# Kernel optimization log

Hardware: AMD Instinct MI355X
Metric: run time of the kernel (lower is better)

Reference implementation:

```python
import jax, jax.numpy as jnp
import numpy as np

TEMPERATURE = 0.5
EPS = 1e-8  # torch.nn.CosineSimilarity default eps


def setup_inputs() -> dict:
    key = jax.random.key(0)
    k1, k2 = jax.random.split(key)
    B, D = 4096, 256
    z1 = jax.random.normal(k1, (B, D), dtype=jnp.float32)
    # z2 = perturbed view of z1 so positive cosine sims are positive
    # (original torch code takes log of the RAW cosine sim, which is NaN
    #  for negative positives; realistic SimCLR positives are correlated views)
    z2 = z1 + 0.1 * jax.random.normal(k2, (B, D), dtype=jnp.float32)
    return {"z1": z1, "z2": z2}


def reference(z1, z2):
    B = z1.shape[0]
    z = jnp.concatenate([z1, z2], axis=0)                      # [2B, D]
    norm = jnp.maximum(jnp.linalg.norm(z, axis=-1, keepdims=True), EPS)
    zn = z / norm
    sim = zn @ zn.T                                            # [2B, 2B] cosine sims
    # positives: sim[i, i+B] and sim[i+B, i] (RAW cosine, per original code)
    pos = jnp.concatenate([jnp.diagonal(sim, offset=B),
                           jnp.diagonal(sim, offset=-B)])      # [2B]
    # mask self-similarity diagonal to -inf before exp-sum
    diag = jnp.eye(2 * B, dtype=bool)
    sim_masked = jnp.where(diag, -jnp.inf, sim)
    denom = jnp.sum(jnp.exp(sim_masked / TEMPERATURE), axis=-1)  # [2B]
    loss = -jnp.mean(jnp.log(pos / denom))
    return loss
```

## Files before the change

kernel.cpp:

```cpp
#include <hip/hip_runtime.h>
#include <hip/hip_bf16.h>


#define NROWS 8192
#define BHALF 4096
#define DDIM  256
#define CHUNK 4

typedef __attribute__((ext_vector_type(4))) int   i32x4;
typedef __attribute__((ext_vector_type(8))) int   i32x8;
typedef __attribute__((ext_vector_type(4))) float f32x4;

#define SCALE1 0x7F7F7F7F
#define TWO_LOG2E 2.8853900817779268f

__device__ __forceinline__ void load_lds16(const unsigned char* g, unsigned char* l) {
    __builtin_amdgcn_global_load_lds(
        (const __attribute__((address_space(1))) void*)g,
        (__attribute__((address_space(3))) void*)l, 16, 0, 0);
}

__global__ __launch_bounds__(256) void prep_kernel(const float* __restrict__ z1,
                                                   const float* __restrict__ z2,
                                                   unsigned char* __restrict__ zn8,
                                                   float* __restrict__ posPart,
                                                   float* __restrict__ denom,
                                                   float* __restrict__ out) {
    __shared__ float sp[4];
    int wave = threadIdx.x >> 6;
    int lane = threadIdx.x & 63;
    int i    = blockIdx.x * 4 + wave;
    float4 a = reinterpret_cast<const float4*>(z1 + (size_t)i * DDIM)[lane];
    float4 b = reinterpret_cast<const float4*>(z2 + (size_t)i * DDIM)[lane];
    float ss1 = a.x * a.x + a.y * a.y + a.z * a.z + a.w * a.w;
    float ss2 = b.x * b.x + b.y * b.y + b.z * b.z + b.w * b.w;
    float dd  = a.x * b.x + a.y * b.y + a.z * b.z + a.w * b.w;
    #pragma unroll
    for (int off = 32; off; off >>= 1) {
        ss1 += __shfl_xor(ss1, off);
        ss2 += __shfl_xor(ss2, off);
        dd  += __shfl_xor(dd, off);
    }
    float n1 = fmaxf(sqrtf(ss1), 1e-8f);
    float n2 = fmaxf(sqrtf(ss2), 1e-8f);
    float i1 = 1.0f / n1, i2 = 1.0f / n2;
    int pa = __builtin_amdgcn_cvt_pk_fp8_f32(a.x * i1, a.y * i1, 0, 0);
    pa     = __builtin_amdgcn_cvt_pk_fp8_f32(a.z * i1, a.w * i1, pa, 1);
    int pb = __builtin_amdgcn_cvt_pk_fp8_f32(b.x * i2, b.y * i2, 0, 0);
    pb     = __builtin_amdgcn_cvt_pk_fp8_f32(b.z * i2, b.w * i2, pb, 1);
    reinterpret_cast<int*>(zn8 + (size_t)i * DDIM)[lane] = pa;
    reinterpret_cast<int*>(zn8 + (size_t)(i + BHALF) * DDIM)[lane] = pb;
    if (lane == 0) sp[wave] = __logf(dd * i1 * i2);
    if (threadIdx.x < 8) denom[blockIdx.x * 8 + threadIdx.x] = 0.0f;
    if (blockIdx.x == 0 && threadIdx.x == 64) out[0] = 0.0f;
    __syncthreads();
    if (threadIdx.x == 0)
        posPart[blockIdx.x] = sp[0] + sp[1] + sp[2] + sp[3];
}

__global__ __launch_bounds__(256, 2) void denom_kernel(const unsigned char* __restrict__ zn8,
                                                       float* __restrict__ denom) {
    __shared__ __align__(16) unsigned char sA[128 * DDIM];
    __shared__ __align__(16) unsigned char sB[2][64 * DDIM];

    int bi  = blockIdx.y;
    int bj0 = bi + blockIdx.x * CHUNK;
    if (bj0 > 63) return;
    int bjEnd = min(bj0 + CHUNK, 64);
    int S = 2 * (bjEnd - bj0);
    int iBase = bi * 128;

    int t    = threadIdx.x;
    int lane = t & 63;
    int wave = t >> 6;
    int col  = lane & 15;
    int quad = lane >> 4;
    int wm = wave >> 1, wn = wave & 1;

    int rowL  = t >> 4;
    int chunk = (t & 15) ^ rowL;

    {
        const unsigned char* gA = zn8 + (size_t)(iBase + rowL) * DDIM + chunk * 16;
        unsigned char* lA = sA + t * 16;
        #pragma unroll
        for (int q = 0; q < 8; q++)
            load_lds16(gA + q * 4096, lA + q * 4096);
        const unsigned char* gB = zn8 + (size_t)(bj0 * 128 + rowL) * DDIM + chunk * 16;
        unsigned char* lB = sB[0] + t * 16;
        #pragma unroll
        for (int q = 0; q < 4; q++)
            load_lds16(gB + q * 4096, lB + q * 4096);
    }

    i32x8 af[4][2];
    float rs[4][4];
    #pragma unroll
    for (int mt = 0; mt < 4; mt++)
        #pragma unroll
        for (int r = 0; r < 4; r++) rs[mt][r] = 0.f;

    const unsigned char* aRow = sA + (size_t)(wm * 64 + col) * DDIM;

    for (int s = 0; s < S; s++) {
        __syncthreads();

        if (s + 1 < S) {
            int bj = bj0 + ((s + 1) >> 1), h = (s + 1) & 1;
            const unsigned char* gB =
                zn8 + (size_t)(bj * 128 + h * 64 + rowL) * DDIM + chunk * 16;
            unsigned char* lB = sB[(s + 1) & 1] + t * 16;
            #pragma unroll
            for (int q = 0; q < 4; q++)
                load_lds16(gB + q * 4096, lB + q * 4096);
        }

        if (s == 0) {
            #pragma unroll
            for (int mt = 0; mt < 4; mt++)
                #pragma unroll
                for (int ks = 0; ks < 2; ks++) {
                    int g0 = ks * 8 + quad * 2;
                    i32x4 lo = *(const i32x4*)(aRow + mt * 16 * DDIM + ((g0    ) ^ col) * 16);
                    i32x4 hi = *(const i32x4*)(aRow + mt * 16 * DDIM + ((g0 + 1) ^ col) * 16);
                    af[mt][ks] = __builtin_shufflevector(lo, hi, 0, 1, 2, 3, 4, 5, 6, 7);
                }
        }

        int bj = bj0 + (s >> 1), h = s & 1;
        int jBase = bj * 128;
        bool isDiag = (bj == bi);
        const unsigned char* bRow = sB[s & 1] + (size_t)(wn * 32 + col) * DDIM;

        i32x8 bfr[2][2];
        #pragma unroll
        for (int nt = 0; nt < 2; nt++)
            #pragma unroll
            for (int ks = 0; ks < 2; ks++) {
                int g0 = ks * 8 + quad * 2;
                i32x4 lo = *(const i32x4*)(bRow + nt * 16 * DDIM + ((g0    ) ^ col) * 16);
                i32x4 hi = *(const i32x4*)(bRow + nt * 16 * DDIM + ((g0 + 1) ^ col) * 16);
                bfr[nt][ks] = __builtin_shufflevector(lo, hi, 0, 1, 2, 3, 4, 5, 6, 7);
            }

        float cs[2] = {0.f, 0.f};
        #pragma unroll
        for (int mt = 0; mt < 4; mt++) {
            int gi = iBase + wm * 64 + mt * 16;
            #pragma unroll
            for (int nt = 0; nt < 2; nt++) {
                f32x4 acc = {0.f, 0.f, 0.f, 0.f};
                acc = __builtin_amdgcn_mfma_scale_f32_16x16x128_f8f6f4(
                          af[mt][0], bfr[nt][0], acc, 0, 0, 0, SCALE1, 0, SCALE1);
                acc = __builtin_amdgcn_mfma_scale_f32_16x16x128_f8f6f4(
                          af[mt][1], bfr[nt][1], acc, 0, 0, 0, SCALE1, 0, SCALE1);
                bool dtile = (gi == jBase + h * 64 + wn * 32 + nt * 16);
                float csl = 0.f;
                #pragma unroll
                for (int r = 0; r < 4; r++) {
                    float e = exp2f(acc[r] * TWO_LOG2E);
                    if (dtile && (quad * 4 + r) == col) e = 0.f;
                    rs[mt][r] += e;
                    csl += e;
                }
                cs[nt] += csl;
            }
        }

        if (!isDiag) {
            #pragma unroll
            for (int nt = 0; nt < 2; nt++) {
                float v = cs[nt];
                v += __shfl_xor(v, 16);
                v += __shfl_xor(v, 32);
                if (quad == 0)
                    atomicAdd(&denom[jBase + h * 64 + wn * 32 + nt * 16 + col], v);
            }
        }
    }

    #pragma unroll
    for (int mt = 0; mt < 4; mt++)
        #pragma unroll
        for (int r = 0; r < 4; r++) {
            float v = rs[mt][r];
            v += __shfl_xor(v, 1);
            v += __shfl_xor(v, 2);
            v += __shfl_xor(v, 4);
            v += __shfl_xor(v, 8);
            rs[mt][r] = v;
        }
    __syncthreads();
    float* red = (float*)sA;
    if (col == 0) {
        #pragma unroll
        for (int mt = 0; mt < 4; mt++)
            #pragma unroll
            for (int r = 0; r < 4; r++)
                red[wn * 128 + wm * 64 + mt * 16 + quad * 4 + r] = rs[mt][r];
    }
    __syncthreads();
    if (t < 128)
        atomicAdd(&denom[iBase + t], red[t] + red[128 + t]);
}

__global__ __launch_bounds__(256) void loss_kernel(const float* __restrict__ posPart,
                                                   const float* __restrict__ denom,
                                                   float* __restrict__ out) {
    __shared__ float sdata[4];
    int t = threadIdx.x;
    float s = __logf(denom[blockIdx.x * 256 + t]);
    if (t < 32) s -= 2.0f * posPart[blockIdx.x * 32 + t];
    #pragma unroll
    for (int off = 32; off; off >>= 1) s += __shfl_xor(s, off);
    if ((t & 63) == 0) sdata[t >> 6] = s;
    __syncthreads();
    if (t == 0)
        atomicAdd(out, (sdata[0] + sdata[1] + sdata[2] + sdata[3]) * (1.0f / NROWS));
}

extern "C" void kernel_launch(void* const* d_in, const int* in_sizes, int n_in,
                              void* d_out, int out_size, void* d_ws, size_t ws_size,
                              hipStream_t stream) {
    const float* z1 = (const float*)d_in[0];
    const float* z2 = (const float*)d_in[1];

    unsigned char* zn8 = (unsigned char*)d_ws;
    float* denom   = (float*)((char*)d_ws + (size_t)NROWS * DDIM);
    float* posPart = denom + NROWS;

    prep_kernel<<<BHALF / 4, 256, 0, stream>>>(z1, z2, zn8, posPart, denom, (float*)d_out);
    denom_kernel<<<dim3(16, 64), 256, 0, stream>>>(zn8, denom);
    loss_kernel<<<NROWS / 256, 256, 0, stream>>>(posPart, denom, (float*)d_out);
}
```

Before: 98.15 us.

## Shrink LDS to 48KB by aliasing B buffer onto A tile for 3 blocks/CU

Preloads the A-fragments into registers up front, then reuses half of the A tile's shared memory as the second B double-buffer. This cuts LDS per block from 64KB to 48KB so three blocks fit per CU. The chunk size drops from 4 to 3 column tiles, with the grid widened to 22 to match. This trades more blocks and atomics, plus extra barriers, for higher occupancy and better load balance on the triangular work.

```diff
diff --git a/kernel.cpp b/kernel.cpp
--- a/kernel.cpp
+++ b/kernel.cpp
@@ -5,7 +5,6 @@
 #define NROWS 8192
 #define BHALF 4096
 #define DDIM  256
-#define CHUNK 4
 
 typedef __attribute__((ext_vector_type(4))) int   i32x4;
 typedef __attribute__((ext_vector_type(8))) int   i32x8;
@@ -58,16 +57,18 @@
         posPart[blockIdx.x] = sp[0] + sp[1] + sp[2] + sp[3];
 }
 
-__global__ __launch_bounds__(256, 2) void denom_kernel(const unsigned char* __restrict__ zn8,
+__global__ __launch_bounds__(256, 3) void denom_kernel(const unsigned char* __restrict__ zn8,
                                                        float* __restrict__ denom) {
-    __shared__ __align__(16) unsigned char sA[128 * DDIM];
-    __shared__ __align__(16) unsigned char sB[2][64 * DDIM];
+    __shared__ __align__(16) unsigned char sMem[48 * 1024];
+    unsigned char* sA   = sMem;
+    unsigned char* buf0 = sMem + 32768;
+    unsigned char* buf1 = sMem + 16384;
 
     int bi  = blockIdx.y;
-    int bj0 = bi + blockIdx.x * CHUNK;
+    int bj0 = bi + blockIdx.x * 3;
     if (bj0 > 63) return;
-    int bjEnd = min(bj0 + CHUNK, 64);
-    int S = 2 * (bjEnd - bj0);
+    int ntiles = min(3, 64 - bj0);
+    int S = 2 * ntiles;
     int iBase = bi * 128;
 
     int t    = threadIdx.x;
@@ -82,55 +83,55 @@
 
     {
         const unsigned char* gA = zn8 + (size_t)(iBase + rowL) * DDIM + chunk * 16;
-        unsigned char* lA = sA + t * 16;
         #pragma unroll
         for (int q = 0; q < 8; q++)
-            load_lds16(gA + q * 4096, lA + q * 4096);
+            load_lds16(gA + q * 4096, sA + t * 16 + q * 4096);
         const unsigned char* gB = zn8 + (size_t)(bj0 * 128 + rowL) * DDIM + chunk * 16;
-        unsigned char* lB = sB[0] + t * 16;
         #pragma unroll
         for (int q = 0; q < 4; q++)
-            load_lds16(gB + q * 4096, lB + q * 4096);
-    }
+            load_lds16(gB + q * 4096, buf0 + t * 16 + q * 4096);
+    }
+    __syncthreads();
 
     i32x8 af[4][2];
+    {
+        const unsigned char* aRow = sA + (size_t)(wm * 64 + col) * DDIM;
+        #pragma unroll
+        for (int mt = 0; mt < 4; mt++)
+            #pragma unroll
+            for (int ks = 0; ks < 2; ks++) {
+                int g0 = ks * 8 + quad * 2;
+                i32x4 lo = *(const i32x4*)(aRow + mt * 16 * DDIM + ((g0    ) ^ col) * 16);
+                i32x4 hi = *(const i32x4*)(aRow + mt * 16 * DDIM + ((g0 + 1) ^ col) * 16);
+                af[mt][ks] = __builtin_shufflevector(lo, hi, 0, 1, 2, 3, 4, 5, 6, 7);
+            }
+    }
+    __syncthreads();
+
     float rs[4][4];
     #pragma unroll
     for (int mt = 0; mt < 4; mt++)
         #pragma unroll
         for (int r = 0; r < 4; r++) rs[mt][r] = 0.f;
 
-    const unsigned char* aRow = sA + (size_t)(wm * 64 + col) * DDIM;
-
     for (int s = 0; s < S; s++) {
-        __syncthreads();
+        if (s) __syncthreads();
 
         if (s + 1 < S) {
-            int bj = bj0 + ((s + 1) >> 1), h = (s + 1) & 1;
-            const unsigned char* gB =
-                zn8 + (size_t)(bj * 128 + h * 64 + rowL) * DDIM + chunk * 16;
-            unsigned char* lB = sB[(s + 1) & 1] + t * 16;
+            int bjn = bj0 + ((s + 1) >> 1), hn = (s + 1) & 1;
+            const unsigned char* g =
+                zn8 + (size_t)(bjn * 128 + hn * 64 + rowL) * DDIM + chunk * 16;
+            unsigned char* dst = ((s + 1) & 1) ? buf1 : buf0;
             #pragma unroll
             for (int q = 0; q < 4; q++)
-                load_lds16(gB + q * 4096, lB + q * 4096);
-        }
-
-        if (s == 0) {
-            #pragma unroll
-            for (int mt = 0; mt < 4; mt++)
-                #pragma unroll
-                for (int ks = 0; ks < 2; ks++) {
-                    int g0 = ks * 8 + quad * 2;
-                    i32x4 lo = *(const i32x4*)(aRow + mt * 16 * DDIM + ((g0    ) ^ col) * 16);
-                    i32x4 hi = *(const i32x4*)(aRow + mt * 16 * DDIM + ((g0 + 1) ^ col) * 16);
-                    af[mt][ks] = __builtin_shufflevector(lo, hi, 0, 1, 2, 3, 4, 5, 6, 7);
-                }
+                load_lds16(g + q * 4096, dst + t * 16 + q * 4096);
         }
 
         int bj = bj0 + (s >> 1), h = s & 1;
         int jBase = bj * 128;
         bool isDiag = (bj == bi);
-        const unsigned char* bRow = sB[s & 1] + (size_t)(wn * 32 + col) * DDIM;
+        const unsigned char* bRow =
+            (((s & 1) ? buf1 : buf0)) + (size_t)(wn * 32 + col) * DDIM;
 
         i32x8 bfr[2][2];
         #pragma unroll
@@ -190,8 +191,7 @@
             v += __shfl_xor(v, 8);
             rs[mt][r] = v;
         }
-    __syncthreads();
-    float* red = (float*)sA;
+    float* red = (float*)sMem;
     if (col == 0) {
         #pragma unroll
         for (int mt = 0; mt < 4; mt++)
@@ -230,6 +230,6 @@
     float* posPart = denom + NROWS;
 
     prep_kernel<<<BHALF / 4, 256, 0, stream>>>(z1, z2, zn8, posPart, denom, (float*)d_out);
-    denom_kernel<<<dim3(16, 64), 256, 0, stream>>>(zn8, denom);
+    denom_kernel<<<dim3(22, 64), 256, 0, stream>>>(zn8, denom);
     loss_kernel<<<NROWS / 256, 256, 0, stream>>>(posPart, denom, (float*)d_out);
 }
```

Result: faster. 86.35 us (-12.0%).
